# Kernel tuning notes

Hardware: AMD Instinct MI355X
Metric: run time of the kernel (lower is better)

## Reference

```python
import jax, jax.numpy as jnp
import numpy as np

def mish(x):
    return x * jnp.tanh(jax.nn.softplus(x))

def setup_inputs() -> dict:
    ANT, RF, DS, G, B = 64, 8, 8, 16, 4096
    BB_DIM = 2 * RF * DS      # 128
    RF_DIM = 2 * ANT * RF     # 1024
    key = jax.random.key(0)
    ks = jax.random.split(key, 10)
    def lin(kw, kb, i, o):
        lim = 1.0 / np.sqrt(i)
        W = jax.random.uniform(kw, (o, i), jnp.float32, -lim, lim)
        b = jax.random.uniform(kb, (o,), jnp.float32, -lim, lim)
        return W, b
    W_rfbb, b_rfbb = lin(ks[0], ks[1], RF_DIM, BB_DIM)
    W_rfrf, b_rfrf = lin(ks[2], ks[3], RF_DIM, RF_DIM)
    W_bbrf, b_bbrf = lin(ks[4], ks[5], BB_DIM, RF_DIM)
    W_bbbb, b_bbbb = lin(ks[6], ks[7], BB_DIM, BB_DIM)
    BB_feature = jax.random.normal(ks[8], (B, G, BB_DIM), jnp.float32)
    RF_feature = jax.random.normal(ks[9], (B, RF_DIM), jnp.float32)
    return {
        "BB_feature": BB_feature, "RF_feature": RF_feature,
        "W_rfbb": W_rfbb, "b_rfbb": b_rfbb,
        "W_rfrf": W_rfrf, "b_rfrf": b_rfrf,
        "W_bbrf": W_bbrf, "b_bbrf": b_bbrf,
        "W_bbbb": W_bbbb, "b_bbbb": b_bbbb,
    }

def reference(BB_feature, RF_feature, W_rfbb, b_rfbb, W_rfrf, b_rfrf, W_bbrf, b_bbrf, W_bbbb, b_bbbb):
    # mean over subcarrier-group dim
    BB_mean = jnp.mean(BB_feature, axis=-2)                      # [B, BB_DIM]
    RF_to_RF = mish(RF_feature @ W_rfrf.T + b_rfrf)              # [B, RF_DIM]
    RF_to_BB = mish(RF_feature @ W_rfbb.T + b_rfbb)              # [B, BB_DIM]
    BB_to_RF = mish(BB_mean @ W_bbrf.T + b_bbrf)                 # [B, RF_DIM]
    BB_to_BB = mish(jnp.einsum('bgi,oi->bgo', BB_feature, W_bbbb) + b_bbbb)  # [B, G, BB_DIM]
    new_RF = RF_to_RF + BB_to_RF
    new_BB = BB_to_BB + RF_to_BB[:, None, :]
    return (new_BB, new_RF)
```

## Files before the change

kernel.cpp:

```cpp
#include <hip/hip_runtime.h>
#include <hip/hip_bf16.h>

typedef __attribute__((ext_vector_type(8))) short short8;
typedef __attribute__((ext_vector_type(4))) short short4v;
typedef __attribute__((ext_vector_type(4))) float floatx4;

#define BDIM 128
#define RDIM 1024
#define NB   4096
#define NG   16

__device__ __forceinline__ float mishf(float x) {
    float e = __expf(x);
    float t = e * (e + 2.0f);
    float r = x * (t / (t + 2.0f));
    return x > 20.0f ? x : r;
}

__device__ __forceinline__ short8 cvt8v(float4 f0, float4 f1) {
    union { __hip_bfloat162 h; unsigned u; } c0, c1, c2, c3;
    c0.h = __float22bfloat162_rn(make_float2(f0.x, f0.y));
    c1.h = __float22bfloat162_rn(make_float2(f0.z, f0.w));
    c2.h = __float22bfloat162_rn(make_float2(f1.x, f1.y));
    c3.h = __float22bfloat162_rn(make_float2(f1.z, f1.w));
    union { short8 s; unsigned u[4]; } r;
    r.u[0] = c0.u; r.u[1] = c1.u; r.u[2] = c2.u; r.u[3] = c3.u;
    return r.s;
}

__device__ __forceinline__ short4v cvt4v(float4 f) {
    union { __hip_bfloat162 h; unsigned u; } c0, c1;
    c0.h = __float22bfloat162_rn(make_float2(f.x, f.y));
    c1.h = __float22bfloat162_rn(make_float2(f.z, f.w));
    union { short4v s; unsigned u[2]; } r;
    r.u[0] = c0.u; r.u[1] = c1.u;
    return r.s;
}

__device__ __forceinline__ void gld16(const void* g, void* l) {
    __builtin_amdgcn_global_load_lds(
        (const __attribute__((address_space(1))) unsigned int*)g,
        (__attribute__((address_space(3))) unsigned int*)l, 16, 0, 0);
}

#define MFMA(a, b, c) __builtin_amdgcn_mfma_f32_16x16x32_bf16(a, b, c, 0, 0, 0)

#define RF_N     4194304u
#define C1       4194304u
#define C2       5242880u
#define C3       5373952u
#define C4       5505024u
#define CT       5521408u

__global__ void __launch_bounds__(256) k_prep(
    const float* __restrict__ bb, const float* __restrict__ rf,
    const float* __restrict__ Wrfrf, const float* __restrict__ Wrfbb,
    const float* __restrict__ Wbbrf, const float* __restrict__ Wbbbb,
    short* __restrict__ bb_b, short* __restrict__ mean_b, short* __restrict__ rf_b,
    short* __restrict__ wrfrf_b, short* __restrict__ wrfbb_b,
    short* __restrict__ wbbrf_b, short* __restrict__ wbbbb_b)
{
    int bid = blockIdx.x;
    int tid = threadIdx.x;
    if (bid < 512) {
        int b = bid * 8 + (tid >> 5);
        int d = (tid & 31) * 4;
        const float4* p = (const float4*)(bb + (size_t)b * (NG * BDIM) + d);
        short* ob = bb_b + (size_t)b * (NG * BDIM) + d;
        float4 s = {0.f, 0.f, 0.f, 0.f};
        #pragma unroll
        for (int g = 0; g < NG; ++g) {
            float4 v = p[g * (BDIM / 4)];
            s.x += v.x; s.y += v.y; s.z += v.z; s.w += v.w;
            *(short4v*)(ob + g * BDIM) = cvt4v(v);
        }
        s.x *= 0.0625f; s.y *= 0.0625f; s.z *= 0.0625f; s.w *= 0.0625f;
        *(short4v*)(mean_b + (size_t)b * BDIM + d) = cvt4v(s);
    } else {
        size_t t = (size_t)(bid - 512) * 256 + tid;
        for (size_t base = t * 8; base < CT; base += (size_t)512 * 256 * 8) {
            const float* s; short* dst; size_t off;
            if (base < C1)      { s = rf;    dst = rf_b;    off = base; }
            else if (base < C2) { s = Wrfrf; dst = wrfrf_b; off = base - C1; }
            else if (base < C3) { s = Wrfbb; dst = wrfbb_b; off = base - C2; }
            else if (base < C4) { s = Wbbrf; dst = wbbrf_b; off = base - C3; }
            else                { s = Wbbbb; dst = wbbbb_b; off = base - C4; }
            float4 f0 = ((const float4*)(s + off))[0];
            float4 f1 = ((const float4*)(s + off))[1];
            *(short8*)(dst + off) = cvt8v(f0, f1);
        }
    }
}

__global__ void __launch_bounds__(256) k_newrf(
    const short* __restrict__ rfb,
    const short* __restrict__ meanb,
    const short* __restrict__ wrfrfb,
    const float* __restrict__ brfrf,
    const short* __restrict__ wbbrfb,
    const float* __restrict__ bbbrf,
    const short* __restrict__ wrfbbb,
    const float* __restrict__ brfbb,
    float* __restrict__ out,
    float* __restrict__ rf2bb)
{
    __shared__ alignas(16) short As[2][128 * 64];
    __shared__ alignas(16) short Bs[2][64 * 64];
    __shared__ alignas(16) short Ws2[2][16 * 64];
    int tid = threadIdx.x;
    int wave = tid >> 6, lane = tid & 63;
    int r = lane & 15, quad = lane >> 4;
    int wm = (wave & 1) * 64, wn = (wave >> 1) * 32;
    int mt = blockIdx.x >> 4, nt = blockIdx.x & 15;
    int m0 = mt * 128, n0 = nt * 64;
    bool doP = (nt < 8);

    int srow = lane >> 3;
    int scol = ((lane & 7) ^ srow) * 8;

    const short* aB = rfb    + (size_t)(m0 + wave * 32 + srow) * RDIM + scol;
    const short* bB = wrfrfb + (size_t)(n0 + wave * 16 + srow) * RDIM + scol;
    const short* wB = wrfbbb + (size_t)(nt * 16 + srow) * RDIM + scol;

    floatx4 acc1[4][2], acc2[4][2], acc3[4];
    #pragma unroll
    for (int mi = 0; mi < 4; ++mi) {
        acc1[mi][0] = floatx4{0.f,0.f,0.f,0.f}; acc1[mi][1] = acc1[mi][0];
        acc2[mi][0] = acc1[mi][0]; acc2[mi][1] = acc1[mi][0];
        acc3[mi] = acc1[mi][0];
    }

    auto stage1 = [&](int buf, int k) {
        #pragma unroll
        for (int j = 0; j < 4; ++j)
            gld16(aB + (size_t)j * 8 * RDIM + k, &As[buf][(wave * 32 + j * 8) * 64]);
        #pragma unroll
        for (int j = 0; j < 2; ++j)
            gld16(bB + (size_t)j * 8 * RDIM + k, &Bs[buf][(wave * 16 + j * 8) * 64]);
        if (doP && wave == 0) {
            #pragma unroll
            for (int j = 0; j < 2; ++j)
                gld16(wB + (size_t)j * 8 * RDIM + k, &Ws2[buf][j * 8 * 64]);
        }
    };

    stage1(0, 0);
    __syncthreads();

    for (int it = 0; it < 16; ++it) {
        int buf = it & 1;
        if (it < 15) stage1(buf ^ 1, (it + 1) * 64);
        const short* Ac = As[buf];
        const short* Bc = Bs[buf];
        const short* Wc = Ws2[buf];
        #pragma unroll
        for (int kk = 0; kk < 2; ++kk) {
            int sw = (((kk << 2) + quad) ^ (r & 7)) << 3;
            short8 af[4];
            #pragma unroll
            for (int mi = 0; mi < 4; ++mi)
                af[mi] = *(const short8*)&Ac[(wm + mi * 16 + r) * 64 + sw];
            short8 bf0 = *(const short8*)&Bc[(wn + r) * 64 + sw];
            short8 bf1 = *(const short8*)&Bc[(wn + 16 + r) * 64 + sw];
            #pragma unroll
            for (int mi = 0; mi < 4; ++mi) {
                acc1[mi][0] = MFMA(af[mi], bf0, acc1[mi][0]);
                acc1[mi][1] = MFMA(af[mi], bf1, acc1[mi][1]);
            }
            if (doP && (wave & 2) == 0) {
                short8 b2 = *(const short8*)&Wc[r * 64 + sw];
                #pragma unroll
                for (int mi = 0; mi < 4; ++mi) acc3[mi] = MFMA(af[mi], b2, acc3[mi]);
            }
        }
        __syncthreads();
    }

    const short* a2B = meanb  + (size_t)(m0 + wave * 32 + srow) * BDIM + scol;
    const short* b2B = wbbrfb + (size_t)(n0 + wave * 16 + srow) * BDIM + scol;
    auto stage2 = [&](int buf, int k) {
        #pragma unroll
        for (int j = 0; j < 4; ++j)
            gld16(a2B + (size_t)j * 8 * BDIM + k, &As[buf][(wave * 32 + j * 8) * 64]);
        #pragma unroll
        for (int j = 0; j < 2; ++j)
            gld16(b2B + (size_t)j * 8 * BDIM + k, &Bs[buf][(wave * 16 + j * 8) * 64]);
    };
    stage2(0, 0);
    __syncthreads();
    for (int it = 0; it < 2; ++it) {
        int buf = it & 1;
        if (it < 1) stage2(1, 64);
        const short* Ac = As[buf];
        const short* Bc = Bs[buf];
        #pragma unroll
        for (int kk = 0; kk < 2; ++kk) {
            int sw = (((kk << 2) + quad) ^ (r & 7)) << 3;
            short8 af[4];
            #pragma unroll
            for (int mi = 0; mi < 4; ++mi)
                af[mi] = *(const short8*)&Ac[(wm + mi * 16 + r) * 64 + sw];
            short8 bf0 = *(const short8*)&Bc[(wn + r) * 64 + sw];
            short8 bf1 = *(const short8*)&Bc[(wn + 16 + r) * 64 + sw];
            #pragma unroll
            for (int mi = 0; mi < 4; ++mi) {
                acc2[mi][0] = MFMA(af[mi], bf0, acc2[mi][0]);
                acc2[mi][1] = MFMA(af[mi], bf1, acc2[mi][1]);
            }
        }
        __syncthreads();
    }

    #pragma unroll
    for (int nj = 0; nj < 2; ++nj) {
        int col = n0 + wn + nj * 16 + r;
        float b1 = brfrf[col];
        float b2 = bbbrf[col];
        #pragma unroll
        for (int mi = 0; mi < 4; ++mi) {
            #pragma unroll
            for (int g = 0; g < 4; ++g) {
                int row = m0 + wm + mi * 16 + quad * 4 + g;
                out[(size_t)row * RDIM + col] =
                    mishf(acc1[mi][nj][g] + b1) + mishf(acc2[mi][nj][g] + b2);
            }
        }
    }
    if (doP && (wave & 2) == 0) {
        int col = nt * 16 + r;
        float bs = brfbb[col];
        #pragma unroll
        for (int mi = 0; mi < 4; ++mi) {
            #pragma unroll
            for (int g = 0; g < 4; ++g) {
                int row = m0 + wm + mi * 16 + quad * 4 + g;
                rf2bb[(size_t)row * BDIM + col] = mishf(acc3[mi][g] + bs);
            }
        }
    }
}

__global__ void __launch_bounds__(256) k_newbb(
    const short* __restrict__ bbb,
    const short* __restrict__ wb,
    const float* __restrict__ bias,
    const float* __restrict__ rf2bb,
    float* __restrict__ out)
{
    __shared__ alignas(16) short At[128 * 128];
    __shared__ alignas(16) short Wt[128 * 128];
    int tid = threadIdx.x;
    int wave = tid >> 6, lane = tid & 63;
    int r = lane & 15, quad = lane >> 4;
    size_t m0 = (size_t)blockIdx.x * 128;

    int lrow = lane >> 4;
    int lslot = lane & 15;
    #pragma unroll
    for (int j = 0; j < 8; ++j) {
        int row = wave * 32 + j * 4 + lrow;
        int col = ((lslot ^ (row & 7)) << 3);
        gld16(bbb + (m0 + row) * BDIM + col, &At[(wave * 32 + j * 4) * 128]);
        gld16(wb + (size_t)row * BDIM + col,  &Wt[(wave * 32 + j * 4) * 128]);
    }

    floatx4 acc[2][8];
    #pragma unroll
    for (int i = 0; i < 2; ++i)
        #pragma unroll
        for (int j = 0; j < 8; ++j) acc[i][j] = floatx4{0.f,0.f,0.f,0.f};

    __syncthreads();

    #pragma unroll
    for (int kc = 0; kc < 4; ++kc) {
        int sw = (((kc << 2) + quad) ^ (r & 7)) << 3;
        short8 a0 = *(const short8*)&At[(wave * 32 + r) * 128 + sw];
        short8 a1 = *(const short8*)&At[(wave * 32 + 16 + r) * 128 + sw];
        #pragma unroll
        for (int nj = 0; nj < 8; ++nj) {
            short8 b = *(const short8*)&Wt[(nj * 16 + r) * 128 + sw];
            acc[0][nj] = MFMA(a0, b, acc[0][nj]);
            acc[1][nj] = MFMA(a1, b, acc[1][nj]);
        }
    }

    #pragma unroll
    for (int mi = 0; mi < 2; ++mi) {
        #pragma unroll
        for (int nj = 0; nj < 8; ++nj) {
            int col = nj * 16 + r;
            float bs = bias[col];
            #pragma unroll
            for (int g = 0; g < 4; ++g) {
                size_t row = m0 + wave * 32 + mi * 16 + quad * 4 + g;
                out[row * BDIM + col] = mishf(acc[mi][nj][g] + bs) + rf2bb[(row >> 4) * BDIM + col];
            }
        }
    }
}

extern "C" void kernel_launch(void* const* d_in, const int* in_sizes, int n_in,
                              void* d_out, int out_size, void* d_ws, size_t ws_size,
                              hipStream_t stream) {
    const float* BB    = (const float*)d_in[0];
    const float* RF    = (const float*)d_in[1];
    const float* Wrfbb = (const float*)d_in[2];
    const float* brfbb = (const float*)d_in[3];
    const float* Wrfrf = (const float*)d_in[4];
    const float* brfrf = (const float*)d_in[5];
    const float* Wbbrf = (const float*)d_in[6];
    const float* bbbrf = (const float*)d_in[7];
    const float* Wbbbb = (const float*)d_in[8];
    const float* bbbbb = (const float*)d_in[9];

    float* outBB = (float*)d_out;
    float* outRF = outBB + (size_t)NB * NG * BDIM;

    char* w = (char*)d_ws;
    short* mean_b  = (short*)(w);
    short* rf_b    = (short*)(w + 1048576);
    short* wrfrf_b = (short*)(w + 9437184);
    short* wrfbb_b = (short*)(w + 11534336);
    short* wbbrf_b = (short*)(w + 11796480);
    short* wbbbb_b = (short*)(w + 12058624);
    short* bb_b    = (short*)(w + 12091392);
    float* rf2bb   = (float*)(w + 28868608);

    k_prep <<<1024, 256, 0, stream>>>(BB, RF, Wrfrf, Wrfbb, Wbbrf, Wbbbb,
                                      bb_b, mean_b, rf_b, wrfrf_b, wrfbb_b,
                                      wbbrf_b, wbbbb_b);
    k_newrf<<<512, 256, 0, stream>>>(rf_b, mean_b, wrfrf_b, brfrf, wbbrf_b, bbbrf,
                                     wrfbb_b, brfbb, outRF, rf2bb);
    k_newbb<<<512, 256, 0, stream>>>(bb_b, wbbbb_b, bbbbb, rf2bb, outBB);
}
```

Before: 153.0 us.

## Use register-staged padded LDS pipeline, smaller newbb tiles, more prep blocks

The RF GEMM kernel drops direct global-to-LDS loads with XOR swizzle. It now uses register-prefetched double buffering with a padded LDS stride and a K step of 32, two tiles ahead. The BB GEMM kernel halves its row tile to 64, doubling the grid, and hoists the rf2bb broadcast load out of the inner loop. The prep kernel gets three times as many flat-conversion blocks. These changes aim to improve occupancy and latency hiding, at the cost of twice as many loop iterations and barriers in the RF GEMM and twice as many W tile loads in the BB kernel.

```diff
diff --git a/kernel.cpp b/kernel.cpp
--- a/kernel.cpp
+++ b/kernel.cpp
@@ -9,6 +9,7 @@
 #define RDIM 1024
 #define NB   4096
 #define NG   16
+#define LDP  40
 
 __device__ __forceinline__ float mishf(float x) {
     float e = __expf(x);
@@ -45,12 +46,12 @@
 
 #define MFMA(a, b, c) __builtin_amdgcn_mfma_f32_16x16x32_bf16(a, b, c, 0, 0, 0)
 
-#define RF_N     4194304u
 #define C1       4194304u
 #define C2       5242880u
 #define C3       5373952u
 #define C4       5505024u
 #define CT       5521408u
+#define FLATB    1536
 
 __global__ void __launch_bounds__(256) k_prep(
     const float* __restrict__ bb, const float* __restrict__ rf,
@@ -78,7 +79,7 @@
         *(short4v*)(mean_b + (size_t)b * BDIM + d) = cvt4v(s);
     } else {
         size_t t = (size_t)(bid - 512) * 256 + tid;
-        for (size_t base = t * 8; base < CT; base += (size_t)512 * 256 * 8) {
+        for (size_t base = t * 8; base < CT; base += (size_t)FLATB * 256 * 8) {
             const float* s; short* dst; size_t off;
             if (base < C1)      { s = rf;    dst = rf_b;    off = base; }
             else if (base < C2) { s = Wrfrf; dst = wrfrf_b; off = base - C1; }
@@ -104,9 +105,9 @@
     float* __restrict__ out,
     float* __restrict__ rf2bb)
 {
-    __shared__ alignas(16) short As[2][128 * 64];
-    __shared__ alignas(16) short Bs[2][64 * 64];
-    __shared__ alignas(16) short Ws2[2][16 * 64];
+    __shared__ short As[2][128 * LDP];
+    __shared__ short Bs[2][64 * LDP];
+    __shared__ short Ws2[2][16 * LDP];
     int tid = threadIdx.x;
     int wave = tid >> 6, lane = tid & 63;
     int r = lane & 15, quad = lane >> 4;
@@ -115,12 +116,15 @@
     int m0 = mt * 128, n0 = nt * 64;
     bool doP = (nt < 8);
 
-    int srow = lane >> 3;
-    int scol = ((lane & 7) ^ srow) * 8;
-
-    const short* aB = rfb    + (size_t)(m0 + wave * 32 + srow) * RDIM + scol;
-    const short* bB = wrfrfb + (size_t)(n0 + wave * 16 + srow) * RDIM + scol;
-    const short* wB = wrfbbb + (size_t)(nt * 16 + srow) * RDIM + scol;
+    int arow = tid >> 1, akh = (tid & 1) * 16;
+    int brow = tid >> 2, bkq = (tid & 3) * 8;
+    int aidx = arow * LDP + akh;
+    int bidx = brow * LDP + bkq;
+    int widx = (tid >> 2) * LDP + bkq;
+
+    const short* aG = rfb    + (size_t)(m0 + arow) * RDIM + akh;
+    const short* bG = wrfrfb + (size_t)(n0 + brow) * RDIM + bkq;
+    const short* wG = wrfbbb + (size_t)(nt * 16 + (tid >> 2)) * RDIM + bkq;
 
     floatx4 acc1[4][2], acc2[4][2], acc3[4];
     #pragma unroll
@@ -129,84 +133,93 @@
         acc2[mi][0] = acc1[mi][0]; acc2[mi][1] = acc1[mi][0];
         acc3[mi] = acc1[mi][0];
     }
-
-    auto stage1 = [&](int buf, int k) {
-        #pragma unroll
-        for (int j = 0; j < 4; ++j)
-            gld16(aB + (size_t)j * 8 * RDIM + k, &As[buf][(wave * 32 + j * 8) * 64]);
-        #pragma unroll
-        for (int j = 0; j < 2; ++j)
-            gld16(bB + (size_t)j * 8 * RDIM + k, &Bs[buf][(wave * 16 + j * 8) * 64]);
-        if (doP && wave == 0) {
+    short8 ra0, ra1, rb0, rw0;
+    bool wload = doP && (tid < 64);
+
+    ra0 = ((const short8*)aG)[0]; ra1 = ((const short8*)aG)[1];
+    rb0 = ((const short8*)bG)[0];
+    if (wload) rw0 = ((const short8*)wG)[0];
+    *(short8*)&As[0][aidx]     = ra0;
+    *(short8*)&As[0][aidx + 8] = ra1;
+    *(short8*)&Bs[0][bidx]     = rb0;
+    if (wload) *(short8*)&Ws2[0][widx] = rw0;
+    ra0 = ((const short8*)(aG + 32))[0]; ra1 = ((const short8*)(aG + 32))[1];
+    rb0 = ((const short8*)(bG + 32))[0];
+    if (wload) rw0 = ((const short8*)(wG + 32))[0];
+    __syncthreads();
+
+    for (int it = 0; it < 32; ++it) {
+        const short* Ac = As[it & 1];
+        const short* Bc = Bs[it & 1];
+        const short* Wc = Ws2[it & 1];
+        short8 af[4];
+        #pragma unroll
+        for (int mi = 0; mi < 4; ++mi)
+            af[mi] = *(const short8*)&Ac[(wm + mi * 16 + r) * LDP + quad * 8];
+        short8 bf[2];
+        bf[0] = *(const short8*)&Bc[(wn + r) * LDP + quad * 8];
+        bf[1] = *(const short8*)&Bc[(wn + 16 + r) * LDP + quad * 8];
+        #pragma unroll
+        for (int mi = 0; mi < 4; ++mi) {
+            acc1[mi][0] = MFMA(af[mi], bf[0], acc1[mi][0]);
+            acc1[mi][1] = MFMA(af[mi], bf[1], acc1[mi][1]);
+        }
+        if (doP && (wave & 2) == 0) {
+            short8 b2 = *(const short8*)&Wc[r * LDP + quad * 8];
             #pragma unroll
-            for (int j = 0; j < 2; ++j)
-                gld16(wB + (size_t)j * 8 * RDIM + k, &Ws2[buf][j * 8 * 64]);
-        }
-    };
-
-    stage1(0, 0);
+            for (int mi = 0; mi < 4; ++mi) acc3[mi] = MFMA(af[mi], b2, acc3[mi]);
+        }
+        if (it < 31) {
+            int nb = (it + 1) & 1;
+            *(short8*)&As[nb][aidx]     = ra0;
+            *(short8*)&As[nb][aidx + 8] = ra1;
+            *(short8*)&Bs[nb][bidx]     = rb0;
+            if (wload) *(short8*)&Ws2[nb][widx] = rw0;
+        }
+        if (it < 30) {
+            int k = (it + 2) * 32;
+            ra0 = ((const short8*)(aG + k))[0]; ra1 = ((const short8*)(aG + k))[1];
+            rb0 = ((const short8*)(bG + k))[0];
+            if (wload) rw0 = ((const short8*)(wG + k))[0];
+        }
+        __syncthreads();
+    }
+
+    const short* a2G = meanb  + (size_t)(m0 + arow) * BDIM + akh;
+    const short* b2G = wbbrfb + (size_t)(n0 + brow) * BDIM + bkq;
+    ra0 = ((const short8*)a2G)[0]; ra1 = ((const short8*)a2G)[1];
+    rb0 = ((const short8*)b2G)[0];
+    *(short8*)&As[0][aidx]     = ra0;
+    *(short8*)&As[0][aidx + 8] = ra1;
+    *(short8*)&Bs[0][bidx]     = rb0;
+    ra0 = ((const short8*)(a2G + 32))[0]; ra1 = ((const short8*)(a2G + 32))[1];
+    rb0 = ((const short8*)(b2G + 32))[0];
     __syncthreads();
-
-    for (int it = 0; it < 16; ++it) {
-        int buf = it & 1;
-        if (it < 15) stage1(buf ^ 1, (it + 1) * 64);
-        const short* Ac = As[buf];
-        const short* Bc = Bs[buf];
-        const short* Wc = Ws2[buf];
-        #pragma unroll
-        for (int kk = 0; kk < 2; ++kk) {
-            int sw = (((kk << 2) + quad) ^ (r & 7)) << 3;
-            short8 af[4];
-            #pragma unroll
-            for (int mi = 0; mi < 4; ++mi)
-                af[mi] = *(const short8*)&Ac[(wm + mi * 16 + r) * 64 + sw];
-            short8 bf0 = *(const short8*)&Bc[(wn + r) * 64 + sw];
-            short8 bf1 = *(const short8*)&Bc[(wn + 16 + r) * 64 + sw];
-            #pragma unroll
-            for (int mi = 0; mi < 4; ++mi) {
-                acc1[mi][0] = MFMA(af[mi], bf0, acc1[mi][0]);
-                acc1[mi][1] = MFMA(af[mi], bf1, acc1[mi][1]);
-            }
-            if (doP && (wave & 2) == 0) {
-                short8 b2 = *(const short8*)&Wc[r * 64 + sw];
-                #pragma unroll
-                for (int mi = 0; mi < 4; ++mi) acc3[mi] = MFMA(af[mi], b2, acc3[mi]);
-            }
-        }
-        __syncthreads();
-    }
-
-    const short* a2B = meanb  + (size_t)(m0 + wave * 32 + srow) * BDIM + scol;
-    const short* b2B = wbbrfb + (size_t)(n0 + wave * 16 + srow) * BDIM + scol;
-    auto stage2 = [&](int buf, int k) {
-        #pragma unroll
-        for (int j = 0; j < 4; ++j)
-            gld16(a2B + (size_t)j * 8 * BDIM + k, &As[buf][(wave * 32 + j * 8) * 64]);
-        #pragma unroll
-        for (int j = 0; j < 2; ++j)
-            gld16(b2B + (size_t)j * 8 * BDIM + k, &Bs[buf][(wave * 16 + j * 8) * 64]);
-    };
-    stage2(0, 0);
-    __syncthreads();
-    for (int it = 0; it < 2; ++it) {
-        int buf = it & 1;
-        if (it < 1) stage2(1, 64);
-        const short* Ac = As[buf];
-        const short* Bc = Bs[buf];
-        #pragma unroll
-        for (int kk = 0; kk < 2; ++kk) {
-            int sw = (((kk << 2) + quad) ^ (r & 7)) << 3;
-            short8 af[4];
-            #pragma unroll
-            for (int mi = 0; mi < 4; ++mi)
-                af[mi] = *(const short8*)&Ac[(wm + mi * 16 + r) * 64 + sw];
-            short8 bf0 = *(const short8*)&Bc[(wn + r) * 64 + sw];
-            short8 bf1 = *(const short8*)&Bc[(wn + 16 + r) * 64 + sw];
-            #pragma unroll
-            for (int mi = 0; mi < 4; ++mi) {
-                acc2[mi][0] = MFMA(af[mi], bf0, acc2[mi][0]);
-                acc2[mi][1] = MFMA(af[mi], bf1, acc2[mi][1]);
-            }
+    for (int it = 0; it < 4; ++it) {
+        const short* Ac = As[it & 1];
+        const short* Bc = Bs[it & 1];
+        short8 af[4];
+        #pragma unroll
+        for (int mi = 0; mi < 4; ++mi)
+            af[mi] = *(const short8*)&Ac[(wm + mi * 16 + r) * LDP + quad * 8];
+        short8 bf[2];
+        bf[0] = *(const short8*)&Bc[(wn + r) * LDP + quad * 8];
+        bf[1] = *(const short8*)&Bc[(wn + 16 + r) * LDP + quad * 8];
+        #pragma unroll
+        for (int mi = 0; mi < 4; ++mi) {
+            acc2[mi][0] = MFMA(af[mi], bf[0], acc2[mi][0]);
+            acc2[mi][1] = MFMA(af[mi], bf[1], acc2[mi][1]);
+        }
+        if (it < 3) {
+            int nb = (it + 1) & 1;
+            *(short8*)&As[nb][aidx]     = ra0;
+            *(short8*)&As[nb][aidx + 8] = ra1;
+            *(short8*)&Bs[nb][bidx]     = rb0;
+        }
+        if (it < 2) {
+            int k = (it + 2) * 32;
+            ra0 = ((const short8*)(a2G + k))[0]; ra1 = ((const short8*)(a2G + k))[1];
+            rb0 = ((const short8*)(b2G + k))[0];
         }
         __syncthreads();
     }
@@ -247,12 +260,12 @@
     const float* __restrict__ rf2bb,
     float* __restrict__ out)
 {
-    __shared__ alignas(16) short At[128 * 128];
+    __shared__ alignas(16) short At[64 * 128];
     __shared__ alignas(16) short Wt[128 * 128];
     int tid = threadIdx.x;
     int wave = tid >> 6, lane = tid & 63;
     int r = lane & 15, quad = lane >> 4;
-    size_t m0 = (size_t)blockIdx.x * 128;
+    size_t m0 = (size_t)blockIdx.x * 64;
 
     int lrow = lane >> 4;
     int lslot = lane & 15;
@@ -260,42 +273,43 @@
     for (int j = 0; j < 8; ++j) {
         int row = wave * 32 + j * 4 + lrow;
         int col = ((lslot ^ (row & 7)) << 3);
-        gld16(bbb + (m0 + row) * BDIM + col, &At[(wave * 32 + j * 4) * 128]);
-        gld16(wb + (size_t)row * BDIM + col,  &Wt[(wave * 32 + j * 4) * 128]);
-    }
-
-    floatx4 acc[2][8];
-    #pragma unroll
-    for (int i = 0; i < 2; ++i)
-        #pragma unroll
-        for (int j = 0; j < 8; ++j) acc[i][j] = floatx4{0.f,0.f,0.f,0.f};
+        gld16(wb + (size_t)row * BDIM + col, &Wt[(wave * 32 + j * 4) * 128]);
+    }
+    #pragma unroll
+    for (int j = 0; j < 4; ++j) {
+        int row = wave * 16 + j * 4 + lrow;
+        int col = ((lslot ^ (row & 7)) << 3);
+        gld16(bbb + (m0 + row) * BDIM + col, &At[(wave * 16 + j * 4) * 128]);
+    }
+
+    floatx4 acc[8];
+    #pragma unroll
+    for (int j = 0; j < 8; ++j) acc[j] = floatx4{0.f,0.f,0.f,0.f};
+
+    size_t prow = (m0 >> 4) + wave;
 
     __syncthreads();
 
     #pragma unroll
     for (int kc = 0; kc < 4; ++kc) {
         int sw = (((kc << 2) + quad) ^ (r & 7)) << 3;
-        short8 a0 = *(const short8*)&At[(wave * 32 + r) * 128 + sw];
-        short8 a1 = *(const short8*)&At[(wave * 32 + 16 + r) * 128 + sw];
+        short8 a = *(const short8*)&At[(wave * 16 + r) * 128 + sw];
         #pragma unroll
         for (int nj = 0; nj < 8; ++nj) {
             short8 b = *(const short8*)&Wt[(nj * 16 + r) * 128 + sw];
-            acc[0][nj] = MFMA(a0, b, acc[0][nj]);
-            acc[1][nj] = MFMA(a1, b, acc[1][nj]);
-        }
-    }
-
-    #pragma unroll
-    for (int mi = 0; mi < 2; ++mi) {
-        #pragma unroll
-        for (int nj = 0; nj < 8; ++nj) {
-            int col = nj * 16 + r;
-            float bs = bias[col];
-            #pragma unroll
-            for (int g = 0; g < 4; ++g) {
-                size_t row = m0 + wave * 32 + mi * 16 + quad * 4 + g;
-                out[row * BDIM + col] = mishf(acc[mi][nj][g] + bs) + rf2bb[(row >> 4) * BDIM + col];
-            }
+            acc[nj] = MFMA(a, b, acc[nj]);
+        }
+    }
+
+    #pragma unroll
+    for (int nj = 0; nj < 8; ++nj) {
+        int col = nj * 16 + r;
+        float bs = bias[col];
+        float pv = rf2bb[prow * BDIM + col];
+        #pragma unroll
+        for (int g = 0; g < 4; ++g) {
+            size_t row = m0 + wave * 16 + quad * 4 + g;
+            out[row * BDIM + col] = mishf(acc[nj][g] + bs) + pv;
         }
     }
 }
@@ -327,10 +341,10 @@
     short* bb_b    = (short*)(w + 12091392);
     float* rf2bb   = (float*)(w + 28868608);
 
-    k_prep <<<1024, 256, 0, stream>>>(BB, RF, Wrfrf, Wrfbb, Wbbrf, Wbbbb,
-                                      bb_b, mean_b, rf_b, wrfrf_b, wrfbb_b,
-                                      wbbrf_b, wbbbb_b);
+    k_prep <<<512 + FLATB, 256, 0, stream>>>(BB, RF, Wrfrf, Wrfbb, Wbbrf, Wbbbb,
+                                             bb_b, mean_b, rf_b, wrfrf_b, wrfbb_b,
+                                             wbbrf_b, wbbbb_b);
     k_newrf<<<512, 256, 0, stream>>>(rf_b, mean_b, wrfrf_b, brfrf, wbbrf_b, bbbrf,
                                      wrfbb_b, brfbb, outRF, rf2bb);
-    k_newbb<<<512, 256, 0, stream>>>(bb_b, wbbbb_b, bbbbb, rf2bb, outBB);
-}
+    k_newbb<<<1024, 256, 0, stream>>>(bb_b, wbbbb_b, bbbbb, rf2bb, outBB);
+}
```

New measurement: 154.2 us. Within noise of the previous version (+0.8%).
